# Performance work log

Hardware: AMD Instinct MI355X
Metric: run time of the kernel (lower is better)

Reference implementation:

```python
import jax, jax.numpy as jnp
import numpy as np

EMBED_DIM = 1024
NUM_HEADS = 16
HEAD_DIM = EMBED_DIM // NUM_HEADS
SCALE = HEAD_DIM ** -0.5
B, S = 4, 2048


def setup_inputs() -> dict:
    key = jax.random.key(0)
    ks = jax.random.split(key, 11)
    std = EMBED_DIM ** -0.5
    return {
        "query": jax.random.normal(ks[0], (B, S, EMBED_DIM), jnp.float32),
        "key": jax.random.normal(ks[1], (B, S, EMBED_DIM), jnp.float32),
        "value": jax.random.normal(ks[2], (B, S, EMBED_DIM), jnp.float32),
        "Wq": jax.random.normal(ks[3], (EMBED_DIM, EMBED_DIM), jnp.float32) * std,
        "bq": jax.random.normal(ks[4], (EMBED_DIM,), jnp.float32) * 0.01,
        "Wk": jax.random.normal(ks[5], (EMBED_DIM, EMBED_DIM), jnp.float32) * std,
        "bk": jax.random.normal(ks[6], (EMBED_DIM,), jnp.float32) * 0.01,
        "Wv": jax.random.normal(ks[7], (EMBED_DIM, EMBED_DIM), jnp.float32) * std,
        "bv": jax.random.normal(ks[8], (EMBED_DIM,), jnp.float32) * 0.01,
        "Wo": jax.random.normal(ks[9], (EMBED_DIM, EMBED_DIM), jnp.float32) * std,
        "bo": jax.random.normal(ks[10], (EMBED_DIM,), jnp.float32) * 0.01,
    }


def reference(query, key, value, Wq, bq, Wk, bk, Wv, bv, Wo, bo):
    b, s, _ = query.shape
    # torch.nn.Linear: x @ W.T + b
    q = query @ Wq.T + bq
    k = key @ Wk.T + bk
    v = value @ Wv.T + bv
    # [b, h, s, d]
    q = q.reshape(b, s, NUM_HEADS, HEAD_DIM).transpose(0, 2, 1, 3)
    k = k.reshape(b, s, NUM_HEADS, HEAD_DIM).transpose(0, 2, 1, 3)
    v = v.reshape(b, s, NUM_HEADS, HEAD_DIM).transpose(0, 2, 1, 3)
    # explicit scores [b, h, s, s]
    scores = jnp.einsum("bhqd,bhkd->bhqk", q, k) * SCALE
    causal = jnp.tril(jnp.ones((s, s), dtype=bool))  # is_causal=True
    scores = jnp.where(causal, scores, -jnp.inf)
    attn = jax.nn.softmax(scores, axis=-1)
    out = jnp.einsum("bhqk,bhkd->bhqd", attn, v)
    out = out.transpose(0, 2, 1, 3).reshape(b, s, EMBED_DIM)
    return out @ Wo.T + bo
```

## Files before the change

kernel.cpp:

```cpp
#include <hip/hip_runtime.h>


#define E 1024
#define HEADS 16
#define HD 64
#define SEQ 2048
#define BATCH 4
#define MROWS (BATCH * SEQ)

typedef __bf16 bf16x8 __attribute__((ext_vector_type(8)));
typedef __bf16 bf16x2 __attribute__((ext_vector_type(2)));
typedef float f32x4 __attribute__((ext_vector_type(4)));
typedef unsigned short ushort8v __attribute__((ext_vector_type(8)));

typedef __attribute__((address_space(1))) void gvoid;
typedef __attribute__((address_space(3))) void lvoid;

__device__ __forceinline__ void async16(const void* g, void* l) {
  __builtin_amdgcn_global_load_lds((gvoid*)g, (lvoid*)l, 16, 0, 0);
}

__device__ __forceinline__ unsigned short f2bf(float f) {
  union { float f; unsigned int u; } v;
  v.f = f;
  unsigned int r = v.u + 0x7FFFu + ((v.u >> 16) & 1u);
  return (unsigned short)(r >> 16);
}

__device__ __forceinline__ unsigned packbf(float a, float b) {
  bf16x2 t;
  t[0] = (__bf16)a;
  t[1] = (__bf16)b;
  return __builtin_bit_cast(unsigned, t);
}

__device__ __forceinline__ void store_out(unsigned short* p, float v) { *p = f2bf(v); }
__device__ __forceinline__ void store_out(float* p, float v) { *p = v; }

struct CastArgs {
  const float* src[4];
  unsigned short* dst[4];
  int n;
};

__global__ __launch_bounds__(256) void cast_kernel(CastArgs a) {
  const float* s = a.src[blockIdx.z];
  unsigned short* d = a.dst[blockIdx.z];
  const int n = a.n;
  const int stride = gridDim.x * blockDim.x * 4;
  for (int i = (blockIdx.x * blockDim.x + threadIdx.x) * 4; i < n; i += stride) {
    float4 v = *(const float4*)(s + i);
    ushort4 o;
    o.x = f2bf(v.x); o.y = f2bf(v.y); o.z = f2bf(v.z); o.w = f2bf(v.w);
    *(ushort4*)(d + i) = o;
  }
}

template <typename OutT>
__device__ __forceinline__ void gemm_body(const unsigned short* __restrict__ A,
                                          const unsigned short* __restrict__ W,
                                          const float* __restrict__ bias,
                                          OutT* __restrict__ out, float scale) {
  __shared__ unsigned short At[128 * 64];
  __shared__ unsigned short Wt[128 * 64];
  const int tid = threadIdx.x;
  const int lane = tid & 63;
  const int wv = tid >> 6;
  const int wm = wv & 1, wn = wv >> 1;
  const int li = lane & 15, g = lane >> 4;
  const int m0 = blockIdx.x * 128, n0 = blockIdx.y * 128;
  f32x4 acc[4][4] = {};

  for (int k0 = 0; k0 < E; k0 += 64) {
    __syncthreads();
#pragma unroll
    for (int i = 0; i < 4; ++i) {
      int c = tid + 256 * i;
      int row = c >> 3, slot = c & 7;
      int gc = slot ^ (row & 7);
      async16(A + (size_t)(m0 + row) * E + k0 + gc * 8, &At[c * 8]);
      async16(W + (size_t)(n0 + row) * E + k0 + gc * 8, &Wt[c * 8]);
    }
    asm volatile("s_waitcnt vmcnt(0)" ::: "memory");
    __syncthreads();
#pragma unroll
    for (int kk = 0; kk < 2; ++kk) {
      bf16x8 af[4], bfr[4];
#pragma unroll
      for (int mt = 0; mt < 4; ++mt) {
        int r = wm * 64 + mt * 16 + li;
        int slot = (kk * 4 + g) ^ (r & 7);
        af[mt] = *(const bf16x8*)&At[r * 64 + slot * 8];
      }
#pragma unroll
      for (int nt = 0; nt < 4; ++nt) {
        int r = wn * 64 + nt * 16 + li;
        int slot = (kk * 4 + g) ^ (r & 7);
        bfr[nt] = *(const bf16x8*)&Wt[r * 64 + slot * 8];
      }
#pragma unroll
      for (int mt = 0; mt < 4; ++mt)
#pragma unroll
        for (int nt = 0; nt < 4; ++nt)
          acc[mt][nt] =
              __builtin_amdgcn_mfma_f32_16x16x32_bf16(af[mt], bfr[nt], acc[mt][nt], 0, 0, 0);
    }
  }

#pragma unroll
  for (int nt = 0; nt < 4; ++nt) {
    int col = n0 + wn * 64 + nt * 16 + li;
    float bv = bias[col];
#pragma unroll
    for (int mt = 0; mt < 4; ++mt) {
#pragma unroll
      for (int r = 0; r < 4; ++r) {
        int row = m0 + wm * 64 + mt * 16 + g * 4 + r;
        store_out(&out[(size_t)row * E + col], (acc[mt][nt][r] + bv) * scale);
      }
    }
  }
}

struct QkvArgs {
  const unsigned short* A[3];
  const unsigned short* W[3];
  const float* bias[3];
  unsigned short* out[3];
  float scale[3];
};

__global__ __launch_bounds__(256) void gemm_qkv(QkvArgs p) {
  const int z = blockIdx.z;
  gemm_body<unsigned short>(p.A[z], p.W[z], p.bias[z], p.out[z], p.scale[z]);
}

__global__ __launch_bounds__(256) void gemm_out_k(const unsigned short* __restrict__ A,
                                                  const unsigned short* __restrict__ W,
                                                  const float* __restrict__ bias,
                                                  float* __restrict__ out) {
  gemm_body<float>(A, W, bias, out, 1.0f);
}

__global__ __launch_bounds__(256, 3) void flash_kernel(const unsigned short* __restrict__ Qb,
                                                       const unsigned short* __restrict__ Kb,
                                                       const unsigned short* __restrict__ Vb,
                                                       unsigned short* __restrict__ Ob) {
  __shared__ unsigned short Kt[128 * 64];
  __shared__ unsigned short Vt[64 * 128];
  const int qt = 15 - blockIdx.x;
  const int bh = blockIdx.y;
  const int b = bh >> 4, h16 = bh & 15;
  const size_t base = (size_t)b * SEQ * E + (size_t)h16 * HD;
  const unsigned short* Qp = Qb + base;
  const unsigned short* Kp = Kb + base;
  const unsigned short* Vp = Vb + base;
  unsigned short* Op = Ob + base;
  const int tid = threadIdx.x, lane = tid & 63, wv = tid >> 6;
  const int li = lane & 15, g = lane >> 4;
  const int s0 = qt * 128;
  const int slo = ((g & 1) << 5) | li;

  bf16x8 qf[2][2];
#pragma unroll
  for (int mt = 0; mt < 2; ++mt)
#pragma unroll
    for (int kk = 0; kk < 2; ++kk) {
      int row = s0 + wv * 32 + mt * 16 + li;
      qf[mt][kk] = *(const bf16x8*)(Qp + (size_t)row * E + kk * 32 + g * 8);
    }

  f32x4 oacc[4][2] = {};
  float mi[2] = {-1e30f, -1e30f};
  float lsum[2] = {0.0f, 0.0f};

  for (int j = 0; j <= qt; ++j) {
    __syncthreads();
#pragma unroll
    for (int i = 0; i < 4; ++i) {
      int c = tid + 256 * i;
      int row = c >> 3, slot = c & 7;
      int gc = slot ^ (row & 7);
      async16(Kp + (size_t)(j * 128 + row) * E + gc * 8, &Kt[c * 8]);
    }
#pragma unroll
    for (int i = 0; i < 4; ++i) {
      int c = tid + 256 * i;
      int key = c & 127, db = (c >> 7) * 8;
      ushort8v vv = *(const ushort8v*)(Vp + (size_t)(j * 128 + key) * E + db);
#pragma unroll
      for (int jj = 0; jj < 8; ++jj) {
        int n = db + jj;
        int slot = (key >> 3) ^ (n & 15);
        Vt[n * 128 + slot * 8 + (key & 7)] = vv[jj];
      }
    }
    asm volatile("s_waitcnt vmcnt(0)" ::: "memory");
    __syncthreads();

#pragma unroll
    for (int h = 0; h < 2; ++h) {
      if (j == qt && h * 64 > wv * 32 + 31) continue;

      f32x4 sacc[4][2] = {};
#pragma unroll
      for (int kk = 0; kk < 2; ++kk) {
        bf16x8 kf[4];
#pragma unroll
        for (int nt = 0; nt < 4; ++nt) {
          int key = h * 64 + nt * 16 + li;
          int slot = (kk * 4 + g) ^ (key & 7);
          kf[nt] = *(const bf16x8*)&Kt[key * 64 + slot * 8];
        }
#pragma unroll
        for (int nt = 0; nt < 4; ++nt)
#pragma unroll
          for (int mt = 0; mt < 2; ++mt)
            sacc[nt][mt] =
                __builtin_amdgcn_mfma_f32_16x16x32_bf16(kf[nt], qf[mt][kk], sacc[nt][mt], 0, 0, 0);
      }

      if (j == qt && h * 64 + 63 > wv * 32) {
#pragma unroll
        for (int nt = 0; nt < 4; ++nt)
#pragma unroll
          for (int mt = 0; mt < 2; ++mt)
#pragma unroll
            for (int r = 0; r < 4; ++r) {
              int keyg = h * 64 + nt * 16 + g * 4 + r;
              int qg = wv * 32 + mt * 16 + li;
              sacc[nt][mt][r] = (keyg > qg) ? -1e30f : sacc[nt][mt][r];
            }
      }

      float alpha[2];
#pragma unroll
      for (int mt = 0; mt < 2; ++mt) {
        float mx = sacc[0][mt][0];
#pragma unroll
        for (int nt = 0; nt < 4; ++nt)
#pragma unroll
          for (int r = 0; r < 4; ++r) mx = fmaxf(mx, sacc[nt][mt][r]);
        mx = fmaxf(mx, __shfl_xor(mx, 16));
        mx = fmaxf(mx, __shfl_xor(mx, 32));
        float mnew = fmaxf(mi[mt], mx);
        alpha[mt] = __expf(mi[mt] - mnew);
        mi[mt] = mnew;
      }

      unsigned pk[4][2][2];
      float rs[2] = {0.0f, 0.0f};
#pragma unroll
      for (int nt = 0; nt < 4; ++nt)
#pragma unroll
        for (int mt = 0; mt < 2; ++mt) {
          float p0 = __expf(sacc[nt][mt][0] - mi[mt]);
          float p1 = __expf(sacc[nt][mt][1] - mi[mt]);
          float p2 = __expf(sacc[nt][mt][2] - mi[mt]);
          float p3 = __expf(sacc[nt][mt][3] - mi[mt]);
          rs[mt] += (p0 + p1) + (p2 + p3);
          pk[nt][mt][0] = packbf(p0, p1);
          pk[nt][mt][1] = packbf(p2, p3);
        }
#pragma unroll
      for (int mt = 0; mt < 2; ++mt) {
        float s = rs[mt];
        s += __shfl_xor(s, 16);
        s += __shfl_xor(s, 32);
        lsum[mt] = lsum[mt] * alpha[mt] + s;
#pragma unroll
        for (int dt = 0; dt < 4; ++dt) oacc[dt][mt] *= alpha[mt];
      }

#pragma unroll
      for (int kk2 = 0; kk2 < 2; ++kk2) {
        const int kc = h * 2 + kk2;
        bf16x8 vf[4];
#pragma unroll
        for (int dt = 0; dt < 4; ++dt) {
          int d = dt * 16 + li;
          int slot = (kc * 4 + g) ^ (d & 15);
          vf[dt] = *(const bf16x8*)&Vt[d * 128 + slot * 8];
        }
#pragma unroll
        for (int mt = 0; mt < 2; ++mt) {
          int a0 = __shfl((int)pk[kk2 * 2][mt][0], slo);
          int a1 = __shfl((int)pk[kk2 * 2][mt][1], slo);
          int a2 = __shfl((int)pk[kk2 * 2][mt][0], slo + 16);
          int a3 = __shfl((int)pk[kk2 * 2][mt][1], slo + 16);
          int c0 = __shfl((int)pk[kk2 * 2 + 1][mt][0], slo);
          int c1 = __shfl((int)pk[kk2 * 2 + 1][mt][1], slo);
          int c2 = __shfl((int)pk[kk2 * 2 + 1][mt][0], slo + 16);
          int c3 = __shfl((int)pk[kk2 * 2 + 1][mt][1], slo + 16);
          bool hi = (g & 2) != 0;
          uint4 bb;
          bb.x = hi ? c0 : a0;
          bb.y = hi ? c1 : a1;
          bb.z = hi ? c2 : a2;
          bb.w = hi ? c3 : a3;
          bf16x8 pf = __builtin_bit_cast(bf16x8, bb);
#pragma unroll
          for (int dt = 0; dt < 4; ++dt)
            oacc[dt][mt] =
                __builtin_amdgcn_mfma_f32_16x16x32_bf16(vf[dt], pf, oacc[dt][mt], 0, 0, 0);
        }
      }
    }
  }

#pragma unroll
  for (int mt = 0; mt < 2; ++mt) {
    float inv = 1.0f / lsum[mt];
    int row = s0 + wv * 32 + mt * 16 + li;
#pragma unroll
    for (int dt = 0; dt < 4; ++dt) {
      ushort4 w;
      w.x = f2bf(oacc[dt][mt][0] * inv);
      w.y = f2bf(oacc[dt][mt][1] * inv);
      w.z = f2bf(oacc[dt][mt][2] * inv);
      w.w = f2bf(oacc[dt][mt][3] * inv);
      *(ushort4*)(Op + (size_t)row * E + dt * 16 + g * 4) = w;
    }
  }
}

extern "C" void kernel_launch(void* const* d_in, const int* in_sizes, int n_in,
                              void* d_out, int out_size, void* d_ws, size_t ws_size,
                              hipStream_t stream) {
  const float* q  = (const float*)d_in[0];
  const float* k  = (const float*)d_in[1];
  const float* v  = (const float*)d_in[2];
  const float* Wq = (const float*)d_in[3];
  const float* bq = (const float*)d_in[4];
  const float* Wk = (const float*)d_in[5];
  const float* bk = (const float*)d_in[6];
  const float* Wv = (const float*)d_in[7];
  const float* bv = (const float*)d_in[8];
  const float* Wo = (const float*)d_in[9];
  const float* bo = (const float*)d_in[10];

  unsigned short* Xq  = (unsigned short*)d_ws;
  unsigned short* Xk  = Xq + (size_t)MROWS * E;
  unsigned short* Xv  = Xk + (size_t)MROWS * E;
  unsigned short* Wqb = Xv + (size_t)MROWS * E;
  unsigned short* Wkb = Wqb + (size_t)E * E;
  unsigned short* Wvb = Wkb + (size_t)E * E;
  unsigned short* Wob = Wvb + (size_t)E * E;
  unsigned short* Qb  = Wob + (size_t)E * E;
  unsigned short* Kb  = Qb + (size_t)MROWS * E;
  unsigned short* Vb  = Kb + (size_t)MROWS * E;
  unsigned short* Og  = Xq;

  CastArgs ca;
  ca.src[0] = q; ca.src[1] = k; ca.src[2] = v; ca.src[3] = nullptr;
  ca.dst[0] = Xq; ca.dst[1] = Xk; ca.dst[2] = Xv; ca.dst[3] = nullptr;
  ca.n = MROWS * E;
  cast_kernel<<<dim3(1024, 1, 3), 256, 0, stream>>>(ca);

  CastArgs cw;
  cw.src[0] = Wq; cw.src[1] = Wk; cw.src[2] = Wv; cw.src[3] = Wo;
  cw.dst[0] = Wqb; cw.dst[1] = Wkb; cw.dst[2] = Wvb; cw.dst[3] = Wob;
  cw.n = E * E;
  cast_kernel<<<dim3(256, 1, 4), 256, 0, stream>>>(cw);

  QkvArgs p;
  p.A[0] = Xq;  p.A[1] = Xk;  p.A[2] = Xv;
  p.W[0] = Wqb; p.W[1] = Wkb; p.W[2] = Wvb;
  p.bias[0] = bq; p.bias[1] = bk; p.bias[2] = bv;
  p.out[0] = Qb; p.out[1] = Kb; p.out[2] = Vb;
  p.scale[0] = 0.125f; p.scale[1] = 1.0f; p.scale[2] = 1.0f;
  gemm_qkv<<<dim3(64, 8, 3), 256, 0, stream>>>(p);

  flash_kernel<<<dim3(16, 64), 256, 0, stream>>>(Qb, Kb, Vb, Og);

  gemm_out_k<<<dim3(64, 8), 256, 0, stream>>>(Og, Wob, bo, (float*)d_out);
}
```

Measured before the change: 407.6 us.

## Pair causal query tiles per block and double-buffer K/V tiles in LDS

Each flash-attention block now handles two query tiles (p and 15-p), so every block does the same number of causal key tiles and K/V tiles are reused across both. K/V staging is double-buffered: the next tile's K is loaded asynchronously and V is read into registers while the current tile is computed, then V is scattered into LDS afterward. This aims to balance work across blocks and hide global load latency. In exchange, the grid is halved to 512 blocks, LDS use doubles, register pressure rises from the two accumulator sets, and occupancy is lowered to 2 blocks per CU.

```diff
diff --git a/kernel.cpp b/kernel.cpp
--- a/kernel.cpp
+++ b/kernel.cpp
@@ -142,13 +142,13 @@
   gemm_body<float>(A, W, bias, out, 1.0f);
 }
 
-__global__ __launch_bounds__(256, 3) void flash_kernel(const unsigned short* __restrict__ Qb,
+__global__ __launch_bounds__(256, 2) void flash_kernel(const unsigned short* __restrict__ Qb,
                                                        const unsigned short* __restrict__ Kb,
                                                        const unsigned short* __restrict__ Vb,
                                                        unsigned short* __restrict__ Ob) {
-  __shared__ unsigned short Kt[128 * 64];
-  __shared__ unsigned short Vt[64 * 128];
-  const int qt = 15 - blockIdx.x;
+  __shared__ unsigned short Kt[2][128 * 64];
+  __shared__ unsigned short Vt[2][64 * 128];
+  const int p = blockIdx.x;
   const int bh = blockIdx.y;
   const int b = bh >> 4, h16 = bh & 15;
   const size_t base = (size_t)b * SEQ * E + (size_t)h16 * HD;
@@ -158,49 +158,62 @@
   unsigned short* Op = Ob + base;
   const int tid = threadIdx.x, lane = tid & 63, wv = tid >> 6;
   const int li = lane & 15, g = lane >> 4;
-  const int s0 = qt * 128;
+  const int qlo = p, qhi = 15 - p;
   const int slo = ((g & 1) << 5) | li;
 
-  bf16x8 qf[2][2];
+  bf16x8 qfL[2][2], qfH[2][2];
 #pragma unroll
   for (int mt = 0; mt < 2; ++mt)
 #pragma unroll
     for (int kk = 0; kk < 2; ++kk) {
-      int row = s0 + wv * 32 + mt * 16 + li;
-      qf[mt][kk] = *(const bf16x8*)(Qp + (size_t)row * E + kk * 32 + g * 8);
-    }
-
-  f32x4 oacc[4][2] = {};
-  float mi[2] = {-1e30f, -1e30f};
-  float lsum[2] = {0.0f, 0.0f};
-
-  for (int j = 0; j <= qt; ++j) {
-    __syncthreads();
+      int rl = qlo * 128 + wv * 32 + mt * 16 + li;
+      int rh = qhi * 128 + wv * 32 + mt * 16 + li;
+      qfL[mt][kk] = *(const bf16x8*)(Qp + (size_t)rl * E + kk * 32 + g * 8);
+      qfH[mt][kk] = *(const bf16x8*)(Qp + (size_t)rh * E + kk * 32 + g * 8);
+    }
+
+  f32x4 oaL[4][2] = {}, oaH[4][2] = {};
+  float miL[2] = {-1e30f, -1e30f}, lsL[2] = {0.0f, 0.0f};
+  float miH[2] = {-1e30f, -1e30f}, lsH[2] = {0.0f, 0.0f};
+
+  ushort8v vv[4];
+
+  auto loadV = [&](int j) {
+#pragma unroll
+    for (int i = 0; i < 4; ++i) {
+      int c = tid + 256 * i;
+      int key = c & 127, db = (c >> 7) * 8;
+      vv[i] = *(const ushort8v*)(Vp + (size_t)(j * 128 + key) * E + db);
+    }
+  };
+  auto stageK = [&](int j, int buf) {
 #pragma unroll
     for (int i = 0; i < 4; ++i) {
       int c = tid + 256 * i;
       int row = c >> 3, slot = c & 7;
       int gc = slot ^ (row & 7);
-      async16(Kp + (size_t)(j * 128 + row) * E + gc * 8, &Kt[c * 8]);
-    }
+      async16(Kp + (size_t)(j * 128 + row) * E + gc * 8, &Kt[buf][c * 8]);
+    }
+  };
+  auto scatV = [&](int buf) {
 #pragma unroll
     for (int i = 0; i < 4; ++i) {
       int c = tid + 256 * i;
       int key = c & 127, db = (c >> 7) * 8;
-      ushort8v vv = *(const ushort8v*)(Vp + (size_t)(j * 128 + key) * E + db);
 #pragma unroll
       for (int jj = 0; jj < 8; ++jj) {
         int n = db + jj;
         int slot = (key >> 3) ^ (n & 15);
-        Vt[n * 128 + slot * 8 + (key & 7)] = vv[jj];
-      }
-    }
-    asm volatile("s_waitcnt vmcnt(0)" ::: "memory");
-    __syncthreads();
-
+        Vt[buf][n * 128 + slot * 8 + (key & 7)] = vv[i][jj];
+      }
+    }
+  };
+
+  auto compute = [&](const bf16x8 (&qf)[2][2], float (&mi)[2], float (&ls)[2],
+                     f32x4 (&oa)[4][2], bool diag, int buf) {
 #pragma unroll
     for (int h = 0; h < 2; ++h) {
-      if (j == qt && h * 64 > wv * 32 + 31) continue;
+      if (diag && h * 64 > wv * 32 + 31) continue;
 
       f32x4 sacc[4][2] = {};
 #pragma unroll
@@ -210,7 +223,7 @@
         for (int nt = 0; nt < 4; ++nt) {
           int key = h * 64 + nt * 16 + li;
           int slot = (kk * 4 + g) ^ (key & 7);
-          kf[nt] = *(const bf16x8*)&Kt[key * 64 + slot * 8];
+          kf[nt] = *(const bf16x8*)&Kt[buf][key * 64 + slot * 8];
         }
 #pragma unroll
         for (int nt = 0; nt < 4; ++nt)
@@ -220,7 +233,7 @@
                 __builtin_amdgcn_mfma_f32_16x16x32_bf16(kf[nt], qf[mt][kk], sacc[nt][mt], 0, 0, 0);
       }
 
-      if (j == qt && h * 64 + 63 > wv * 32) {
+      if (diag && h * 64 + 63 > wv * 32) {
 #pragma unroll
         for (int nt = 0; nt < 4; ++nt)
 #pragma unroll
@@ -267,9 +280,9 @@
         float s = rs[mt];
         s += __shfl_xor(s, 16);
         s += __shfl_xor(s, 32);
-        lsum[mt] = lsum[mt] * alpha[mt] + s;
-#pragma unroll
-        for (int dt = 0; dt < 4; ++dt) oacc[dt][mt] *= alpha[mt];
+        ls[mt] = ls[mt] * alpha[mt] + s;
+#pragma unroll
+        for (int dt = 0; dt < 4; ++dt) oa[dt][mt] *= alpha[mt];
       }
 
 #pragma unroll
@@ -280,7 +293,7 @@
         for (int dt = 0; dt < 4; ++dt) {
           int d = dt * 16 + li;
           int slot = (kc * 4 + g) ^ (d & 15);
-          vf[dt] = *(const bf16x8*)&Vt[d * 128 + slot * 8];
+          vf[dt] = *(const bf16x8*)&Vt[buf][d * 128 + slot * 8];
         }
 #pragma unroll
         for (int mt = 0; mt < 2; ++mt) {
@@ -301,25 +314,48 @@
           bf16x8 pf = __builtin_bit_cast(bf16x8, bb);
 #pragma unroll
           for (int dt = 0; dt < 4; ++dt)
-            oacc[dt][mt] =
-                __builtin_amdgcn_mfma_f32_16x16x32_bf16(vf[dt], pf, oacc[dt][mt], 0, 0, 0);
+            oa[dt][mt] =
+                __builtin_amdgcn_mfma_f32_16x16x32_bf16(vf[dt], pf, oa[dt][mt], 0, 0, 0);
         }
       }
     }
+  };
+
+  loadV(0);
+  stageK(0, 0);
+  scatV(0);
+
+  for (int j = 0; j <= qhi; ++j) {
+    const int buf = j & 1;
+    asm volatile("s_waitcnt vmcnt(0)" ::: "memory");
+    __syncthreads();
+    if (j < qhi) {
+      loadV(j + 1);
+      stageK(j + 1, buf ^ 1);
+    }
+    compute(qfH, miH, lsH, oaH, j == qhi, buf);
+    if (j <= qlo) compute(qfL, miL, lsL, oaL, j == qlo, buf);
+    if (j < qhi) scatV(buf ^ 1);
   }
 
 #pragma unroll
-  for (int mt = 0; mt < 2; ++mt) {
-    float inv = 1.0f / lsum[mt];
-    int row = s0 + wv * 32 + mt * 16 + li;
-#pragma unroll
-    for (int dt = 0; dt < 4; ++dt) {
-      ushort4 w;
-      w.x = f2bf(oacc[dt][mt][0] * inv);
-      w.y = f2bf(oacc[dt][mt][1] * inv);
-      w.z = f2bf(oacc[dt][mt][2] * inv);
-      w.w = f2bf(oacc[dt][mt][3] * inv);
-      *(ushort4*)(Op + (size_t)row * E + dt * 16 + g * 4) = w;
+  for (int t = 0; t < 2; ++t) {
+    const int qt = t ? qhi : qlo;
+    f32x4(&oa)[4][2] = t ? oaH : oaL;
+    float* ls = t ? lsH : lsL;
+#pragma unroll
+    for (int mt = 0; mt < 2; ++mt) {
+      float inv = 1.0f / ls[mt];
+      int row = qt * 128 + wv * 32 + mt * 16 + li;
+#pragma unroll
+      for (int dt = 0; dt < 4; ++dt) {
+        ushort4 w;
+        w.x = f2bf(oa[dt][mt][0] * inv);
+        w.y = f2bf(oa[dt][mt][1] * inv);
+        w.z = f2bf(oa[dt][mt][2] * inv);
+        w.w = f2bf(oa[dt][mt][3] * inv);
+        *(ushort4*)(Op + (size_t)row * E + dt * 16 + g * 4) = w;
+      }
     }
   }
 }
@@ -371,7 +407,7 @@
   p.scale[0] = 0.125f; p.scale[1] = 1.0f; p.scale[2] = 1.0f;
   gemm_qkv<<<dim3(64, 8, 3), 256, 0, stream>>>(p);
 
-  flash_kernel<<<dim3(16, 64), 256, 0, stream>>>(Qb, Kb, Vb, Og);
+  flash_kernel<<<dim3(8, 64), 256, 0, stream>>>(Qb, Kb, Vb, Og);
 
   gemm_out_k<<<dim3(64, 8), 256, 0, stream>>>(Og, Wob, bo, (float*)d_out);
 }
```

Result: no change. 405.7 us (-0.5%).
